# Optimization experiments

Hardware: AMD Instinct MI355X
Metric: run time of the kernel (lower is better)

## Reference

```python
import jax, jax.numpy as jnp
import numpy as np

N_EMBD = 1024
N_HEAD = 16

def _lin_params(key, fan_in, fan_out):
    kw, kb = jax.random.split(key)
    bound = 1.0 / np.sqrt(fan_in)
    W = jax.random.uniform(kw, (fan_in, fan_out), minval=-bound, maxval=bound, dtype=jnp.float32)
    b = jax.random.uniform(kb, (fan_out,), minval=-bound, maxval=bound, dtype=jnp.float32)
    return W, b

def setup_inputs() -> dict:
    key = jax.random.key(0)
    ks = jax.random.split(key, 6)
    x = jax.random.normal(ks[0], (2, 2048, N_EMBD), dtype=jnp.float32)
    W_attn, b_attn = _lin_params(ks[1], N_EMBD, 3 * N_EMBD)
    W_proj, b_proj = _lin_params(ks[2], N_EMBD, N_EMBD)
    W_fc, b_fc = _lin_params(ks[3], N_EMBD, 4 * N_EMBD)
    W_fc2, b_fc2 = _lin_params(ks[4], 4 * N_EMBD, N_EMBD)
    ln1_g = jnp.ones((N_EMBD,), jnp.float32); ln1_b = jnp.zeros((N_EMBD,), jnp.float32)
    ln2_g = jnp.ones((N_EMBD,), jnp.float32); ln2_b = jnp.zeros((N_EMBD,), jnp.float32)
    return {"x": x, "W_attn": W_attn, "b_attn": b_attn, "W_proj": W_proj, "b_proj": b_proj,
            "W_fc": W_fc, "b_fc": b_fc, "W_fc2": W_fc2, "b_fc2": b_fc2,
            "ln1_g": ln1_g, "ln1_b": ln1_b, "ln2_g": ln2_g, "ln2_b": ln2_b}

def _layernorm(x, g, b, eps=1e-5):
    mu = jnp.mean(x, axis=-1, keepdims=True)
    var = jnp.var(x, axis=-1, keepdims=True)
    return (x - mu) * jax.lax.rsqrt(var + eps) * g + b

def _attention(x, W_attn, b_attn, W_proj, b_proj):
    B, T, C = x.shape
    hd = C // N_HEAD
    qkv = x @ W_attn + b_attn                      # [B,T,3C]
    q, k, v = jnp.split(qkv, 3, axis=-1)
    # [B,T,C] -> [B,H,T,hd]
    q = q.reshape(B, T, N_HEAD, hd).transpose(0, 2, 1, 3)
    k = k.reshape(B, T, N_HEAD, hd).transpose(0, 2, 1, 3)
    v = v.reshape(B, T, N_HEAD, hd).transpose(0, 2, 1, 3)
    att = jnp.einsum('bhqd,bhkd->bhqk', q, k) * (1.0 / np.sqrt(hd))
    causal = jnp.tril(jnp.ones((T, T), bool))
    att = jnp.where(causal[None, None], att, -jnp.inf)
    att = jax.nn.softmax(att, axis=-1)
    y = jnp.einsum('bhqk,bhkd->bhqd', att, v)      # [B,H,T,hd]
    y = y.transpose(0, 2, 1, 3).reshape(B, T, C)
    return y @ W_proj + b_proj

def _mlp(x, W_fc, b_fc, W_fc2, b_fc2):
    h = jax.nn.gelu(x @ W_fc + b_fc, approximate=False)
    return h @ W_fc2 + b_fc2

def reference(x, W_attn, b_attn, W_proj, b_proj, W_fc, b_fc, W_fc2, b_fc2,
              ln1_g, ln1_b, ln2_g, ln2_b):
    x = x + _attention(_layernorm(x, ln1_g, ln1_b), W_attn, b_attn, W_proj, b_proj)
    x = x + _mlp(_layernorm(x, ln2_g, ln2_b), W_fc, b_fc, W_fc2, b_fc2)
    return x
```

## Files before the change

### kernel.cpp

```cpp
#include <hip/hip_runtime.h>
#include <cstdint>
#include <cstddef>


typedef unsigned short u16;
typedef short bf16x8 __attribute__((ext_vector_type(8)));
typedef float f32x4 __attribute__((ext_vector_type(4)));

#define C_EMBD 1024
#define T_SEQ  2048
#define N_BATCH 2
#define N_HEADS 16
#define HEAD_D 64
#define M_TOK  4096
#define Q_SCALE 0.18033688011112042f

__device__ __forceinline__ u16 f2b(float f) {
  union { float f; unsigned u; } v; v.f = f;
  unsigned r = (v.u + 0x7fffu + ((v.u >> 16) & 1u)) >> 16;
  return (u16)r;
}
__device__ __forceinline__ float b2f(u16 u) {
  union { unsigned u; float f; } v; v.u = ((unsigned)u) << 16;
  return v.f;
}
__device__ __forceinline__ unsigned pk2(float a, float b) {
  union { float f; unsigned u; } x, y; x.f = a; y.f = b;
  return __builtin_amdgcn_perm(y.u, x.u, 0x07060302u);
}
__device__ __forceinline__ void load_lds16(const void* g, void* l) {
  __builtin_amdgcn_global_load_lds(
      (const __attribute__((address_space(1))) void*)g,
      (__attribute__((address_space(3))) void*)l, 16, 0, 0);
}
__device__ __forceinline__ float gelu_fast(float x) {
  const float p = x * __builtin_fmaf(0.044715f * x, x, 1.0f);
  const float t = __builtin_amdgcn_exp2f(2.3021859215f * p);
  return x * t * __builtin_amdgcn_rcpf(t + 1.0f);
}

__global__ __launch_bounds__(256) void transpose_cast_all(
    const float* __restrict__ W0, u16* __restrict__ D0,
    const float* __restrict__ W1, u16* __restrict__ D1,
    const float* __restrict__ W2, u16* __restrict__ D2,
    const float* __restrict__ W3, u16* __restrict__ D3) {
  int id = blockIdx.x;
  const float* W; u16* D; int K, N, t;
  if (id < 3072)      { W = W0; D = D0; K = 1024; N = 3072; t = id; }
  else if (id < 4096) { W = W1; D = D1; K = 1024; N = 1024; t = id - 3072; }
  else if (id < 8192) { W = W2; D = D2; K = 1024; N = 4096; t = id - 4096; }
  else                { W = W3; D = D3; K = 4096; N = 1024; t = id - 8192; }
  const int nTN = N >> 5;
  const int n0 = (t % nTN) * 32, k0 = (t / nTN) * 32;
  __shared__ float tile[32][33];
  const int tx = threadIdx.x & 31, ty = threadIdx.x >> 5;
#pragma unroll
  for (int i = 0; i < 32; i += 8)
    tile[ty + i][tx] = W[(size_t)(k0 + ty + i) * N + n0 + tx];
  __syncthreads();
#pragma unroll
  for (int i = 0; i < 32; i += 8)
    D[(size_t)(n0 + ty + i) * K + k0 + tx] = f2b(tile[tx][ty + i]);
}

__global__ __launch_bounds__(256) void ln_cast(
    const float* __restrict__ X, const float* __restrict__ g,
    const float* __restrict__ b, u16* __restrict__ Y) {
  const int row = blockIdx.x;
  const int tid = threadIdx.x;
  const float4 v = ((const float4*)(X + (size_t)row * C_EMBD))[tid];
  float s = v.x + v.y + v.z + v.w;
  float ss = v.x * v.x + v.y * v.y + v.z * v.z + v.w * v.w;
#pragma unroll
  for (int off = 32; off > 0; off >>= 1) {
    s += __shfl_down(s, off, 64);
    ss += __shfl_down(ss, off, 64);
  }
  __shared__ float red[8];
  __shared__ float stats[2];
  const int wave = tid >> 6, lane = tid & 63;
  if (lane == 0) { red[wave] = s; red[4 + wave] = ss; }
  __syncthreads();
  if (tid == 0) {
    float S = red[0] + red[1] + red[2] + red[3];
    float SS = red[4] + red[5] + red[6] + red[7];
    float mu = S * (1.0f / C_EMBD);
    float var = SS * (1.0f / C_EMBD) - mu * mu;
    stats[0] = mu;
    stats[1] = rsqrtf(var + 1e-5f);
  }
  __syncthreads();
  const float mu = stats[0], rs = stats[1];
  const float4 gv = ((const float4*)g)[tid];
  const float4 bv = ((const float4*)b)[tid];
  ushort4 o;
  o.x = f2b((v.x - mu) * rs * gv.x + bv.x);
  o.y = f2b((v.y - mu) * rs * gv.y + bv.y);
  o.z = f2b((v.z - mu) * rs * gv.z + bv.z);
  o.w = f2b((v.w - mu) * rs * gv.w + bv.w);
  ((ushort4*)(Y + (size_t)row * C_EMBD))[tid] = o;
}

__global__ __launch_bounds__(256) void ln_reduce_cast(
    const float* __restrict__ P0, const float* __restrict__ P1,
    const float* __restrict__ bias, const float* __restrict__ res,
    const float* __restrict__ g, const float* __restrict__ b,
    float* __restrict__ X1, u16* __restrict__ Y) {
  const int row = blockIdx.x;
  const int tid = threadIdx.x;
  const size_t base = (size_t)row * C_EMBD;
  const float4 p0 = ((const float4*)(P0 + base))[tid];
  const float4 p1 = ((const float4*)(P1 + base))[tid];
  const float4 rr = ((const float4*)(res + base))[tid];
  const float4 bb = ((const float4*)bias)[tid];
  float4 v;
  v.x = p0.x + p1.x + rr.x + bb.x;
  v.y = p0.y + p1.y + rr.y + bb.y;
  v.z = p0.z + p1.z + rr.z + bb.z;
  v.w = p0.w + p1.w + rr.w + bb.w;
  ((float4*)(X1 + base))[tid] = v;
  float s = v.x + v.y + v.z + v.w;
  float ss = v.x * v.x + v.y * v.y + v.z * v.z + v.w * v.w;
#pragma unroll
  for (int off = 32; off > 0; off >>= 1) {
    s += __shfl_down(s, off, 64);
    ss += __shfl_down(ss, off, 64);
  }
  __shared__ float red[8];
  __shared__ float stats[2];
  const int wave = tid >> 6, lane = tid & 63;
  if (lane == 0) { red[wave] = s; red[4 + wave] = ss; }
  __syncthreads();
  if (tid == 0) {
    float S = red[0] + red[1] + red[2] + red[3];
    float SS = red[4] + red[5] + red[6] + red[7];
    float mu = S * (1.0f / C_EMBD);
    float var = SS * (1.0f / C_EMBD) - mu * mu;
    stats[0] = mu;
    stats[1] = rsqrtf(var + 1e-5f);
  }
  __syncthreads();
  const float mu = stats[0], rs = stats[1];
  const float4 gv = ((const float4*)g)[tid];
  const float4 bv = ((const float4*)b)[tid];
  ushort4 o;
  o.x = f2b((v.x - mu) * rs * gv.x + bv.x);
  o.y = f2b((v.y - mu) * rs * gv.y + bv.y);
  o.z = f2b((v.z - mu) * rs * gv.z + bv.z);
  o.w = f2b((v.w - mu) * rs * gv.w + bv.w);
  ((ushort4*)(Y + base))[tid] = o;
}

enum { EPI_BF16 = 0, EPI_GELU_BF16 = 2, EPI_PART = 3, EPI_QKV = 4 };

template <int EPI, int SPLIT>
__global__ __launch_bounds__(256) void gemm_bt(
    const u16* __restrict__ A, const u16* __restrict__ Bt,
    const float* __restrict__ bias,
    void* __restrict__ Cout, void* __restrict__ Cout2, void* __restrict__ Cout3,
    int M, int N, int K) {
  __shared__ u16 As[128 * 64];
  __shared__ u16 Bs[128 * 64];
  const int tid = threadIdx.x;
  const int wave = tid >> 6, lane = tid & 63;
  const int quad = lane >> 4, l16 = lane & 15;
  const int sw = l16 & 7;

  const int id = (int)blockIdx.y * (int)gridDim.x + (int)blockIdx.x;
  const int mt = ((id & 7) << 2) + ((id >> 3) & 3);
  const int nt_ = id >> 5;
  const int m0 = mt * 128, n0 = nt_ * 128;

  const int wm = (wave >> 1) * 64, wn = (wave & 1) * 64;

  f32x4 acc[4][4] = {};

  size_t aOff[4], bOff[4];
  int ldsOff[4];
#pragma unroll
  for (int i = 0; i < 4; ++i) {
    const int c = tid + i * 256;
    const int row = c >> 3, gc = ((c & 7) ^ (row & 7)) * 8;
    aOff[i] = (size_t)(m0 + row) * K + gc;
    bOff[i] = (size_t)(n0 + row) * K + gc;
    ldsOff[i] = c * 8;
  }

  const int kTiles = (K >> 6) / SPLIT;
  const int kt0 = (SPLIT == 2) ? (int)blockIdx.z * kTiles : 0;
  for (int kt = kt0; kt < kt0 + kTiles; ++kt) {
    const int k0 = kt << 6;
#pragma unroll
    for (int i = 0; i < 4; ++i)
      load_lds16(A + aOff[i] + k0, &As[ldsOff[i]]);
#pragma unroll
    for (int i = 0; i < 4; ++i)
      load_lds16(Bt + bOff[i] + k0, &Bs[ldsOff[i]]);
    __syncthreads();
#pragma unroll
    for (int ks = 0; ks < 2; ++ks) {
      bf16x8 aF[4], bF[4];
#pragma unroll
      for (int t = 0; t < 4; ++t) {
        aF[t] = *(const bf16x8*)
            &As[(wm + t * 16 + l16) * 64 + (((ks * 4 + quad) ^ sw) * 8)];
        bF[t] = *(const bf16x8*)
            &Bs[(wn + t * 16 + l16) * 64 + (((ks * 4 + quad) ^ sw) * 8)];
      }
#pragma unroll
      for (int tm = 0; tm < 4; ++tm)
#pragma unroll
        for (int tn = 0; tn < 4; ++tn)
          acc[tm][tn] = __builtin_amdgcn_mfma_f32_16x16x32_bf16(
              bF[tn], aF[tm], acc[tm][tn], 0, 0, 0);
    }
    __syncthreads();
  }

  float* Pz = (float*)((SPLIT == 2 && blockIdx.z == 1) ? Cout2 : Cout);
#pragma unroll
  for (int tm = 0; tm < 4; ++tm) {
    const int row = m0 + wm + tm * 16 + l16;
#pragma unroll
    for (int tn = 0; tn < 4; ++tn) {
      const int col = n0 + wn + tn * 16 + quad * 4;
      if constexpr (EPI == EPI_PART) {
        *(float4*)&Pz[(size_t)row * N + col] = *(float4*)&acc[tm][tn];
      } else {
        const float4 bz = *(const float4*)&bias[col];
        float v0 = acc[tm][tn][0] + bz.x, v1 = acc[tm][tn][1] + bz.y;
        float v2 = acc[tm][tn][2] + bz.z, v3 = acc[tm][tn][3] + bz.w;
        if constexpr (EPI == EPI_GELU_BF16) {
          v0 = gelu_fast(v0); v1 = gelu_fast(v1);
          v2 = gelu_fast(v2); v3 = gelu_fast(v3);
        }
        ushort4 o;
        o.x = f2b(v0); o.y = f2b(v1); o.z = f2b(v2); o.w = f2b(v3);
        *(ushort4*)&((u16*)Cout)[(size_t)row * N + col] = o;
      }
    }
  }
}

#define G_LOADA(MQ, PAR)                                                      \
  { const u16* Ab_ = &lds[(unsigned)((((MQ)*2 + (PAR))) << 13)];              \
    _Pragma("unroll") for (int t_ = 0; t_ < 4; ++t_)                          \
      _Pragma("unroll") for (int ks = 0; ks < 2; ++ks)                        \
        aF[t_][ks] = *(const bf16x8*)&Ab_[(wm * 64 + t_ * 16 + l16) * 64 +    \
                                          (((ks * 4 + quad) ^ sw) << 3)]; }
#define G_LOADB(BV, NQ, PAR)                                                  \
  { const u16* Bb_ = &lds[(unsigned)(((2 + (NQ)) * 2 + (PAR)) << 13)];        \
    _Pragma("unroll") for (int u_ = 0; u_ < 2; ++u_)                          \
      _Pragma("unroll") for (int ks = 0; ks < 2; ++ks)                        \
        BV[u_][ks] = *(const bf16x8*)&Bb_[(wn * 32 + u_ * 16 + l16) * 64 +    \
                                          (((ks * 4 + quad) ^ sw) << 3)]; }
#define G_MMA(MQ, NQ, BV)                                                     \
    _Pragma("unroll") for (int t_ = 0; t_ < 4; ++t_)                          \
      _Pragma("unroll") for (int u_ = 0; u_ < 2; ++u_)                        \
        _Pragma("unroll") for (int ks = 0; ks < 2; ++ks)                      \
          acc[(MQ)*4 + t_][(NQ)*2 + u_] =                                     \
              __builtin_amdgcn_mfma_f32_16x16x32_bf16(                        \
                  BV[u_][ks], aF[t_][ks], acc[(MQ)*4 + t_][(NQ)*2 + u_],      \
                  0, 0, 0);
#define G_BAR()   __builtin_amdgcn_s_barrier()
#define G_LGKM0() asm volatile("s_waitcnt lgkmcnt(0)" ::: "memory")
#define G_PRIO(x) __builtin_amdgcn_s_setprio(x)

template <int EPI, int SPLIT>
__global__ __launch_bounds__(512, 2) void gemm256(
    const u16* __restrict__ A, const u16* __restrict__ Bt,
    const float* __restrict__ bias,
    void* __restrict__ Cout, void* __restrict__ Cout2,
    void* __restrict__ Cout3, void* __restrict__ Cout4,
    int M, int N, int K) {
  __shared__ u16 lds[8 * 8192];
  const int tid = threadIdx.x;
  const int lane = tid & 63;
  const int wave = tid >> 6;
  const int quad = lane >> 4, l16 = lane & 15;
  const int sw = l16 & 7;
  const int wm = wave >> 2, wn = wave & 3;

  const int nwg = (int)gridDim.x;
  const int rawid = (int)blockIdx.x;
  const int id = (rawid & 7) * (nwg >> 3) + (rawid >> 3);
  const int nTM = M >> 8;
  const int mt = id % nTM, ntl = id / nTM;
  const int m0 = mt << 8, n0 = ntl << 8;

  f32x4 acc[8][4] = {};

  size_t aOffs[2][2], bOffs[2][2];
  int ldsc[2];
#pragma unroll
  for (int i = 0; i < 2; ++i) {
    const int c = tid + i * 512;
    const int r = c >> 3;
    const int scc = ((c & 7) ^ (r & 7)) << 3;
    ldsc[i] = c * 8;
    const int ra = ((r >> 6) << 7) + (r & 63);
    const int rb = ((r >> 5) << 6) + (r & 31);
    aOffs[0][i] = (size_t)(m0 + ra) * K + scc;
    aOffs[1][i] = (size_t)(m0 + ra + 64) * K + scc;
    bOffs[0][i] = (size_t)(n0 + rb) * K + scc;
    bOffs[1][i] = (size_t)(n0 + rb + 32) * K + scc;
  }
  auto stA = [&](int mq, int p, int kt) {
    u16* dst = &lds[(size_t)((mq * 2 + p) << 13)];
    const int k0 = kt << 6;
#pragma unroll
    for (int i = 0; i < 2; ++i)
      load_lds16(A + aOffs[mq][i] + k0, dst + ldsc[i]);
  };
  auto stB = [&](int nq, int p, int kt) {
    u16* dst = &lds[(size_t)(((2 + nq) * 2 + p) << 13)];
    const int k0 = kt << 6;
#pragma unroll
    for (int i = 0; i < 2; ++i)
      load_lds16(Bt + bOffs[nq][i] + k0, dst + ldsc[i]);
  };

  const int NT = (K >> 6) / SPLIT;
  const int kt0 = (SPLIT > 1) ? (int)blockIdx.z * NT : 0;

  stA(0, 0, kt0); stB(0, 0, kt0); stA(1, 0, kt0); stB(1, 0, kt0);
  stB(0, 1, kt0 + 1); stA(0, 1, kt0 + 1);
  asm volatile("s_waitcnt vmcnt(4)" ::: "memory");
  G_BAR();

  bf16x8 aF[4][2];
  bf16x8 bF0[2][2], bF1[2][2];

  for (int t = 0; t < NT; t += 2) {
#pragma unroll
    for (int p = 0; p < 2; ++p) {
      const int par = p;
      const int k1 = kt0 + (t + 1 + p < NT ? t + 1 + p : 0);
      const int k2 = kt0 + (t + 2 + p < NT ? t + 2 + p : 0);
      G_LOADA(0, par); G_LOADB(bF0, 0, par);
      stA(1, par ^ 1, k1);
      G_BAR(); G_LGKM0(); G_PRIO(1); G_MMA(0, 0, bF0); G_PRIO(0); G_BAR();
      G_LOADB(bF1, 1, par);
      stB(1, par ^ 1, k1);
      G_BAR(); G_LGKM0(); G_PRIO(1); G_MMA(0, 1, bF1); G_PRIO(0); G_BAR();
      G_LOADA(1, par);
      stA(0, par, k2);
      G_BAR(); G_LGKM0(); G_PRIO(1); G_MMA(1, 0, bF0); G_PRIO(0); G_BAR();
      stB(0, par, k2);
      G_BAR(); G_PRIO(1); G_MMA(1, 1, bF1); G_PRIO(0);
      asm volatile("s_waitcnt vmcnt(4)" ::: "memory");
      G_BAR();
    }
  }
  asm volatile("s_waitcnt vmcnt(0)" ::: "memory");

  if constexpr (EPI == EPI_PART) {
    const int z = (SPLIT > 1) ? (int)blockIdx.z : 0;
    float* Pz = (float*)(z == 0 ? Cout : z == 1 ? Cout2
                                       : z == 2 ? Cout3 : Cout4);
#pragma unroll
    for (int tm = 0; tm < 8; ++tm) {
      const int row = m0 + wm * 128 + tm * 16 + l16;
#pragma unroll
      for (int tn = 0; tn < 4; ++tn) {
        const int col = n0 + wn * 64 + tn * 16 + quad * 4;
        *(float4*)&Pz[(size_t)row * N + col] = *(float4*)&acc[tm][tn];
      }
    }
  } else if constexpr (EPI == EPI_QKV) {
#pragma unroll
    for (int tm = 0; tm < 8; ++tm) {
      const int row = m0 + wm * 128 + tm * 16 + l16;
      const int bb = row >> 11, tt = row & (T_SEQ - 1);
#pragma unroll
      for (int tn = 0; tn < 4; ++tn) {
        const int col = n0 + wn * 64 + tn * 16 + quad * 4;
        const float4 bz = *(const float4*)&bias[col];
        float v0 = acc[tm][tn][0] + bz.x, v1 = acc[tm][tn][1] + bz.y;
        float v2 = acc[tm][tn][2] + bz.z, v3 = acc[tm][tn][3] + bz.w;
        const int sec = col >> 10;
        const int h = (col & 1023) >> 6, d4 = col & 63;
        const int bh = bb * N_HEADS + h;
        if (sec == 0) {
          ushort4 o;
          o.x = f2b(v0 * Q_SCALE); o.y = f2b(v1 * Q_SCALE);
          o.z = f2b(v2 * Q_SCALE); o.w = f2b(v3 * Q_SCALE);
          *(ushort4*)&((u16*)Cout)[((size_t)bh * T_SEQ + tt) * HEAD_D + d4] = o;
        } else if (sec == 1) {
          ushort4 o;
          o.x = f2b(v0); o.y = f2b(v1); o.z = f2b(v2); o.w = f2b(v3);
          *(ushort4*)&((u16*)Cout2)[((size_t)bh * T_SEQ + tt) * HEAD_D + d4] = o;
        } else {
          u16* vp = (u16*)Cout3 + ((size_t)bh * HEAD_D + d4) * T_SEQ + tt;
          vp[0] = f2b(v0); vp[T_SEQ] = f2b(v1);
          vp[2 * T_SEQ] = f2b(v2); vp[3 * T_SEQ] = f2b(v3);
        }
      }
    }
  } else {
#pragma unroll
    for (int tm = 0; tm < 8; ++tm) {
      const int row = m0 + wm * 128 + tm * 16 + l16;
#pragma unroll
      for (int tn = 0; tn < 4; ++tn) {
        const int col = n0 + wn * 64 + tn * 16 + quad * 4;
        const float4 bz = *(const float4*)&bias[col];
        float v0 = acc[tm][tn][0] + bz.x, v1 = acc[tm][tn][1] + bz.y;
        float v2 = acc[tm][tn][2] + bz.z, v3 = acc[tm][tn][3] + bz.w;
        if constexpr (EPI == EPI_GELU_BF16) {
          v0 = gelu_fast(v0); v1 = gelu_fast(v1);
          v2 = gelu_fast(v2); v3 = gelu_fast(v3);
        }
        ushort4 o;
        o.x = f2b(v0); o.y = f2b(v1); o.z = f2b(v2); o.w = f2b(v3);
        *(ushort4*)&((u16*)Cout)[(size_t)row * N + col] = o;
      }
    }
  }
}

__global__ __launch_bounds__(256) void reduce_add4(
    const float* __restrict__ P0, const float* __restrict__ P1,
    const float* __restrict__ P2, const float* __restrict__ P3,
    const float* __restrict__ bias, const float* __restrict__ res,
    float* __restrict__ out) {
  const int idx = blockIdx.x * 256 + threadIdx.x;
  const float4 a = ((const float4*)P0)[idx];
  const float4 b = ((const float4*)P1)[idx];
  const float4 c = ((const float4*)P2)[idx];
  const float4 d = ((const float4*)P3)[idx];
  const float4 r = ((const float4*)res)[idx];
  const float4 g = ((const float4*)bias)[idx & 255];
  float4 o;
  o.x = a.x + b.x + c.x + d.x + r.x + g.x;
  o.y = a.y + b.y + c.y + d.y + r.y + g.y;
  o.z = a.z + b.z + c.z + d.z + r.z + g.z;
  o.w = a.w + b.w + c.w + d.w + r.w + g.w;
  ((float4*)out)[idx] = o;
}

__global__ __launch_bounds__(256, 4) void attn_fwd(
    const u16* __restrict__ Q, const u16* __restrict__ Kb,
    const u16* __restrict__ Vt, u16* __restrict__ Y) {
  const int id = (int)blockIdx.x;
  const int xcd = id & 7, slot = id >> 3;
  const int bh = xcd + ((slot & 3) << 3);
  const int qb = (T_SEQ / 64 - 1) - (slot >> 2);
  const int tid = threadIdx.x;
  const int wave = tid >> 6, lane = tid & 63;
  const int quad = lane >> 4, l16 = lane & 15;
  const int sw = l16 & 7;
  const u16* Qp = Q + (size_t)bh * T_SEQ * HEAD_D;
  const u16* Kp = Kb + (size_t)bh * T_SEQ * HEAD_D;
  const u16* Vp = Vt + (size_t)bh * HEAD_D * T_SEQ;

  __shared__ u16 Ks[2][64 * 64];
  __shared__ u16 Vs[2][64 * 64];
  __shared__ u16 Pl[4][16 * 64];

  const int c1 = tid, c2 = tid + 256;
  const int r1 = c1 >> 3, g1 = ((c1 & 7) ^ (r1 & 7)) * 8;
  const int r2 = c2 >> 3, g2 = ((c2 & 7) ^ (r2 & 7)) * 8;
  const size_t kO1 = (size_t)r1 * HEAD_D + g1, kO2 = (size_t)r2 * HEAD_D + g2;
  const size_t vO1 = (size_t)r1 * T_SEQ + g1, vO2 = (size_t)r2 * T_SEQ + g2;
  u16* const dK1[2] = {&Ks[0][c1 * 8], &Ks[1][c1 * 8]};
  u16* const dK2[2] = {&Ks[0][c2 * 8], &Ks[1][c2 * 8]};
  u16* const dV1[2] = {&Vs[0][c1 * 8], &Vs[1][c1 * 8]};
  u16* const dV2[2] = {&Vs[0][c2 * 8], &Vs[1][c2 * 8]};

  auto stageK = [&](int bb, int k0) {
    const u16* base = Kp + (size_t)k0 * HEAD_D;
    load_lds16(base + kO1, dK1[bb]);
    load_lds16(base + kO2, dK2[bb]);
  };
  auto stageV = [&](int bb, int k0) {
    const u16* base = Vp + k0;
    load_lds16(base + vO1, dV1[bb]);
    load_lds16(base + vO2, dV2[bb]);
  };

  const int b = bh >> 4, h = bh & 15;
  const int q0 = qb * 64;
  const int qglob = q0 + wave * 16 + l16;

  bf16x8 qF[2];
  qF[0] = *(const bf16x8*)&Qp[(size_t)qglob * HEAD_D + quad * 8];
  qF[1] = *(const bf16x8*)&Qp[(size_t)qglob * HEAD_D + 32 + quad * 8];

  f32x4 o[4] = {};
  float mrun = -3e38f, lrun = 0.0f;

  stageK(0, 0);
  stageV(0, 0);

  int buf = 0;
  for (int kb = 0; kb <= qb; ++kb) {
    const int k0 = kb * 64;
    __syncthreads();
    if (kb < qb) {
      stageK(buf ^ 1, k0 + 64);
      stageV(buf ^ 1, k0 + 64);
    }
    f32x4 st[4] = {};
#pragma unroll
    for (int ks = 0; ks < 2; ++ks) {
#pragma unroll
      for (int nt = 0; nt < 4; ++nt) {
        bf16x8 kF = *(const bf16x8*)
            &Ks[buf][(nt * 16 + l16) * 64 + (((ks * 4 + quad) ^ sw) * 8)];
        st[nt] = __builtin_amdgcn_mfma_f32_16x16x32_bf16(kF, qF[ks], st[nt],
                                                         0, 0, 0);
      }
    }
    if (kb == qb) {
#pragma unroll
      for (int nt = 0; nt < 4; ++nt) {
#pragma unroll
        for (int r = 0; r < 4; ++r) {
          const int key = k0 + nt * 16 + quad * 4 + r;
          if (key > qglob) st[nt][r] = -3e38f;
        }
      }
    }
    float m = st[0][0];
#pragma unroll
    for (int nt = 0; nt < 4; ++nt)
#pragma unroll
      for (int r = 0; r < 4; ++r) m = fmaxf(m, st[nt][r]);
    m = fmaxf(m, __shfl_xor(m, 16, 64));
    m = fmaxf(m, __shfl_xor(m, 32, 64));
    if (!__all(m - mrun <= 8.0f)) {
      const float nm = fmaxf(mrun, m);
      const float alpha = __builtin_amdgcn_exp2f(mrun - nm);
      mrun = nm;
      lrun *= alpha;
#pragma unroll
      for (int nt = 0; nt < 4; ++nt)
#pragma unroll
        for (int r = 0; r < 4; ++r) o[nt][r] *= alpha;
    }
    float sum = 0.0f;
#pragma unroll
    for (int nt = 0; nt < 4; ++nt)
#pragma unroll
      for (int r = 0; r < 4; ++r) {
        const float p = __builtin_amdgcn_exp2f(st[nt][r] - mrun);
        st[nt][r] = p;
        sum += p;
      }
    sum += __shfl_xor(sum, 16, 64);
    sum += __shfl_xor(sum, 32, 64);
    lrun += sum;
#pragma unroll
    for (int nt = 0; nt < 4; ++nt) {
      uint2 pk;
      pk.x = pk2(st[nt][0], st[nt][1]);
      pk.y = pk2(st[nt][2], st[nt][3]);
      const int wc = (((2 * nt + (quad >> 1)) ^ sw) << 3) + ((quad & 1) << 2);
      *(uint2*)&Pl[wave][(l16 << 6) + wc] = pk;
    }
#pragma unroll
    for (int ks = 0; ks < 2; ++ks) {
      bf16x8 aP = *(const bf16x8*)
          &Pl[wave][(l16 << 6) + (((ks * 4 + quad) ^ sw) << 3)];
#pragma unroll
      for (int nt = 0; nt < 4; ++nt) {
        bf16x8 vF = *(const bf16x8*)
            &Vs[buf][(nt * 16 + l16) * 64 + (((ks * 4 + quad) ^ sw) * 8)];
        o[nt] =
            __builtin_amdgcn_mfma_f32_16x16x32_bf16(vF, aP, o[nt], 0, 0, 0);
      }
    }
    buf ^= 1;
  }

  const float rl = 1.0f / lrun;
  u16* yp = Y + ((size_t)(b * T_SEQ + qglob)) * C_EMBD + h * HEAD_D;
#pragma unroll
  for (int nt = 0; nt < 4; ++nt) {
    ushort4 ov;
    ov.x = f2b(o[nt][0] * rl); ov.y = f2b(o[nt][1] * rl);
    ov.z = f2b(o[nt][2] * rl); ov.w = f2b(o[nt][3] * rl);
    *(ushort4*)&yp[nt * 16 + quad * 4] = ov;
  }
}

extern "C" void kernel_launch(void* const* d_in, const int* in_sizes, int n_in,
                              void* d_out, int out_size, void* d_ws,
                              size_t ws_size, hipStream_t stream) {
  const float* x      = (const float*)d_in[0];
  const float* W_attn = (const float*)d_in[1];
  const float* b_attn = (const float*)d_in[2];
  const float* W_proj = (const float*)d_in[3];
  const float* b_proj = (const float*)d_in[4];
  const float* W_fc   = (const float*)d_in[5];
  const float* b_fc   = (const float*)d_in[6];
  const float* W_fc2  = (const float*)d_in[7];
  const float* b_fc2  = (const float*)d_in[8];
  const float* ln1_g  = (const float*)d_in[9];
  const float* ln1_b  = (const float*)d_in[10];
  const float* ln2_g  = (const float*)d_in[11];
  const float* ln2_b  = (const float*)d_in[12];

  u16* wfc2T = (u16*)d_ws;
  float* x1  = (float*)(wfc2T + (size_t)1024 * 4096);
  u16* hbuf  = (u16*)(x1 + (size_t)M_TOK * C_EMBD);
  u16* dead  = hbuf + (size_t)M_TOK * 4096;
  u16* wqkvT = dead;
  u16* wprojT = wqkvT + (size_t)3072 * 1024;
  u16* wfcT  = wprojT + (size_t)1024 * 1024;
  u16* Abuf  = wfcT + (size_t)4096 * 1024;
  u16* Qb    = Abuf + (size_t)M_TOK * C_EMBD;
  u16* Kbuf  = Qb + (size_t)32 * T_SEQ * HEAD_D;
  u16* Vtb   = Kbuf + (size_t)32 * T_SEQ * HEAD_D;

  float* projP = (float*)hbuf;
  float* fc2P1 = (float*)dead;
  float* fc2P2 = fc2P1 + (size_t)M_TOK * C_EMBD;
  float* fc2P3 = fc2P2 + (size_t)M_TOK * C_EMBD;

  const dim3 blk(256);
  const dim3 blk512(512);

  transpose_cast_all<<<12288, blk, 0, stream>>>(
      W_attn, wqkvT, W_proj, wprojT, W_fc, wfcT, W_fc2, wfc2T);

  ln_cast<<<M_TOK, blk, 0, stream>>>(x, ln1_g, ln1_b, Abuf);

  gemm256<EPI_QKV, 1><<<dim3(192), blk512, 0, stream>>>(
      Abuf, wqkvT, b_attn, Qb, Kbuf, Vtb, nullptr, M_TOK, 3072, 1024);

  attn_fwd<<<dim3(1024), blk, 0, stream>>>(Qb, Kbuf, Vtb, Abuf);

  gemm_bt<EPI_PART, 2><<<dim3(1024 / 128, M_TOK / 128, 2), blk, 0, stream>>>(
      Abuf, wprojT, nullptr, projP, projP + (size_t)M_TOK * C_EMBD, nullptr,
      M_TOK, 1024, 1024);
  ln_reduce_cast<<<M_TOK, blk, 0, stream>>>(
      projP, projP + (size_t)M_TOK * C_EMBD, b_proj, x, ln2_g, ln2_b,
      x1, Abuf);

  gemm256<EPI_GELU_BF16, 1><<<dim3(256), blk512, 0, stream>>>(
      Abuf, wfcT, b_fc, hbuf, nullptr, nullptr, nullptr, M_TOK, 4096, 1024);

  gemm256<EPI_PART, 4><<<dim3(64, 1, 4), blk512, 0, stream>>>(
      hbuf, wfc2T, nullptr, d_out, fc2P1, fc2P2, fc2P3, M_TOK, 1024, 4096);
  reduce_add4<<<M_TOK * C_EMBD / 1024, blk, 0, stream>>>(
      (const float*)d_out, fc2P1, fc2P2, fc2P3, b_fc2, x1, (float*)d_out);
}
```

Before: 324.0 us.

## Double-buffer LDS fragments in gemm256 and regroup tile mapping per XCD

Restructures the 256x256 GEMM main loop so the next A/B fragments are read from LDS into separate register sets while the current MFMA block runs. This removes most barriers and the explicit lgkmcnt(0) waits between phases. It also replaces the block-id-to-tile mapping with an XCD-aware grouped layout that uses a serpentine order for L2 reuse. The extra fragment registers raise register pressure, and the changed barrier and waitcnt placement risks LDS races.

After: 364.8 us. 1.13x slower.

```diff
diff --git a/kernel.cpp b/kernel.cpp
--- a/kernel.cpp
+++ b/kernel.cpp
@@ -242,28 +242,28 @@
   }
 }
 
-#define G_LOADA(MQ, PAR)                                                      \
+#define G_LOADA(DST, MQ, PAR)                                                 \
   { const u16* Ab_ = &lds[(unsigned)((((MQ)*2 + (PAR))) << 13)];              \
     _Pragma("unroll") for (int t_ = 0; t_ < 4; ++t_)                          \
       _Pragma("unroll") for (int ks = 0; ks < 2; ++ks)                        \
-        aF[t_][ks] = *(const bf16x8*)&Ab_[(wm * 64 + t_ * 16 + l16) * 64 +    \
-                                          (((ks * 4 + quad) ^ sw) << 3)]; }
-#define G_LOADB(BV, NQ, PAR)                                                  \
+        DST[t_][ks] = *(const bf16x8*)&Ab_[(wm * 64 + t_ * 16 + l16) * 64 +   \
+                                           (((ks * 4 + quad) ^ sw) << 3)]; }
+#define G_LOADB(DST, NQ, PAR)                                                 \
   { const u16* Bb_ = &lds[(unsigned)(((2 + (NQ)) * 2 + (PAR)) << 13)];        \
     _Pragma("unroll") for (int u_ = 0; u_ < 2; ++u_)                          \
       _Pragma("unroll") for (int ks = 0; ks < 2; ++ks)                        \
-        BV[u_][ks] = *(const bf16x8*)&Bb_[(wn * 32 + u_ * 16 + l16) * 64 +    \
-                                          (((ks * 4 + quad) ^ sw) << 3)]; }
-#define G_MMA(MQ, NQ, BV)                                                     \
+        DST[u_][ks] = *(const bf16x8*)&Bb_[(wn * 32 + u_ * 16 + l16) * 64 +   \
+                                           (((ks * 4 + quad) ^ sw) << 3)]; }
+#define G_MMA(MQ, NQ, AV, BV)                                                 \
     _Pragma("unroll") for (int t_ = 0; t_ < 4; ++t_)                          \
       _Pragma("unroll") for (int u_ = 0; u_ < 2; ++u_)                        \
         _Pragma("unroll") for (int ks = 0; ks < 2; ++ks)                      \
           acc[(MQ)*4 + t_][(NQ)*2 + u_] =                                     \
               __builtin_amdgcn_mfma_f32_16x16x32_bf16(                        \
-                  BV[u_][ks], aF[t_][ks], acc[(MQ)*4 + t_][(NQ)*2 + u_],      \
+                  BV[u_][ks], AV[t_][ks], acc[(MQ)*4 + t_][(NQ)*2 + u_],      \
                   0, 0, 0);
 #define G_BAR()   __builtin_amdgcn_s_barrier()
-#define G_LGKM0() asm volatile("s_waitcnt lgkmcnt(0)" ::: "memory")
+#define G_VM4()   asm volatile("s_waitcnt vmcnt(4)" ::: "memory")
 #define G_PRIO(x) __builtin_amdgcn_s_setprio(x)
 
 template <int EPI, int SPLIT>
@@ -281,11 +281,17 @@
   const int sw = l16 & 7;
   const int wm = wave >> 2, wn = wave & 3;
 
-  const int nwg = (int)gridDim.x;
-  const int rawid = (int)blockIdx.x;
-  const int id = (rawid & 7) * (nwg >> 3) + (rawid >> 3);
-  const int nTM = M >> 8;
-  const int mt = id % nTM, ntl = id / nTM;
+  const int nTM = M >> 8, nTN = N >> 8;
+  const int xcd = (int)blockIdx.x & 7;
+  const int s = (int)blockIdx.x >> 3;
+  const int gn = (nTN >= 6) ? 2 : 1;
+  const int gm = 8 / gn;
+  const int am = nTM / gm, bn = nTN / gn;
+  const int bi = s / am;
+  int ai = s % am;
+  if (bi & 1) ai = am - 1 - ai;
+  const int mt = (xcd % gm) * am + ai;
+  const int ntl = (xcd / gm) * bn + bi;
   const int m0 = mt << 8, n0 = ntl << 8;
 
   f32x4 acc[8][4] = {};
@@ -323,13 +329,15 @@
   const int NT = (K >> 6) / SPLIT;
   const int kt0 = (SPLIT > 1) ? (int)blockIdx.z * NT : 0;
 
-  stA(0, 0, kt0); stB(0, 0, kt0); stA(1, 0, kt0); stB(1, 0, kt0);
-  stB(0, 1, kt0 + 1); stA(0, 1, kt0 + 1);
-  asm volatile("s_waitcnt vmcnt(4)" ::: "memory");
+  bf16x8 aF0[4][2], aF1[4][2];
+  bf16x8 bF0[2][2], bF1[2][2];
+
+  stA(1, 0, kt0); stB(1, 0, kt0); stA(0, 0, kt0); stB(0, 0, kt0);
+  stA(0, 1, kt0 + 1); stB(0, 1, kt0 + 1);
+  G_VM4();
   G_BAR();
-
-  bf16x8 aF[4][2];
-  bf16x8 bF0[2][2], bF1[2][2];
+  G_LOADA(aF0, 0, 0);
+  G_LOADB(bF0, 0, 0);
 
   for (int t = 0; t < NT; t += 2) {
 #pragma unroll
@@ -337,18 +345,23 @@
       const int par = p;
       const int k1 = kt0 + (t + 1 + p < NT ? t + 1 + p : 0);
       const int k2 = kt0 + (t + 2 + p < NT ? t + 2 + p : 0);
-      G_LOADA(0, par); G_LOADB(bF0, 0, par);
+      G_LOADB(bF1, 1, par);
       stA(1, par ^ 1, k1);
-      G_BAR(); G_LGKM0(); G_PRIO(1); G_MMA(0, 0, bF0); G_PRIO(0); G_BAR();
-      G_LOADB(bF1, 1, par);
+      G_PRIO(1); G_MMA(0, 0, aF0, bF0); G_PRIO(0);
+      G_BAR();
+      G_LOADA(aF1, 1, par);
       stB(1, par ^ 1, k1);
-      G_BAR(); G_LGKM0(); G_PRIO(1); G_MMA(0, 1, bF1); G_PRIO(0); G_BAR();
-      G_LOADA(1, par);
+      G_PRIO(1); G_MMA(0, 1, aF0, bF1); G_PRIO(0);
+      G_VM4();
+      G_BAR();
+      G_LOADA(aF0, 0, par ^ 1);
       stA(0, par, k2);
-      G_BAR(); G_LGKM0(); G_PRIO(1); G_MMA(1, 0, bF0); G_PRIO(0); G_BAR();
+      G_PRIO(1); G_MMA(1, 0, aF1, bF0); G_PRIO(0);
+      G_BAR();
+      G_LOADB(bF0, 0, par ^ 1);
       stB(0, par, k2);
-      G_BAR(); G_PRIO(1); G_MMA(1, 1, bF1); G_PRIO(0);
-      asm volatile("s_waitcnt vmcnt(4)" ::: "memory");
+      G_PRIO(1); G_MMA(1, 1, aF1, bF1); G_PRIO(0);
+      G_VM4();
       G_BAR();
     }
   }
```
